# Kernel optimization log

Measured on AMD Instinct MI355X. Metric: run time of the kernel, lower is better.

The kernel has to match this reference:

```python
import jax, jax.numpy as jnp
import numpy as np

B, T, D = 4, 2048, 1024
H, DH = 16, 64
GH = H * DH  # == D here
SCALE = DH ** -0.5
LN_EPS = 1e-5


def setup_inputs() -> dict:
    key = jax.random.key(0)
    ks = jax.random.split(key, 8)
    x = jax.random.normal(ks[0], (B, T, D), dtype=jnp.float32)
    attn_mask = jax.random.uniform(ks[1], (T, T), dtype=jnp.float32)
    # LayerNorm params
    gamma = jnp.ones((D,), jnp.float32)
    beta = jnp.zeros((D,), jnp.float32)
    # projection weights, stored (in, out) so y = x @ W
    Wq = jax.random.normal(ks[2], (D, GH), jnp.float32) * (D ** -0.5)
    Wk = jax.random.normal(ks[3], (D, GH), jnp.float32) * (D ** -0.5)
    Wv = jax.random.normal(ks[4], (D, GH), jnp.float32) * (D ** -0.5)
    Wo = jax.random.normal(ks[5], (GH, D), jnp.float32) * (GH ** -0.5)
    bo = jnp.zeros((D,), jnp.float32)
    return {"x": x, "attn_mask": attn_mask, "gamma": gamma, "beta": beta,
            "Wq": Wq, "Wk": Wk, "Wv": Wv, "Wo": Wo, "bo": bo}


def reference(x, attn_mask, gamma, beta, Wq, Wk, Wv, Wo, bo):
    # LayerNorm over last dim
    mu = jnp.mean(x, axis=-1, keepdims=True)
    var = jnp.mean((x - mu) ** 2, axis=-1, keepdims=True)
    xn = (x - mu) * jax.lax.rsqrt(var + LN_EPS) * gamma + beta
    # QKV projections (bias=False), reshape to [B, H, T, DH]
    split = lambda y: y.reshape(B, T, H, DH).transpose(0, 2, 1, 3)
    q = split(xn @ Wq)
    k = split(xn @ Wk)
    v = split(xn @ Wv)
    # scores scaled then MULTIPLICATIVELY masked (post-scale)
    scores = jnp.einsum('bhqd,bhkd->bhqk', q, k) * SCALE
    scores = scores * attn_mask  # broadcast [T,T] over [B,H,T,T]
    probs = jax.nn.softmax(scores, axis=-1)  # dropout p=0 -> identity
    av = jnp.einsum('bhqk,bhkd->bhqd', probs, v)
    av = av.transpose(0, 2, 1, 3).reshape(B, T, GH)
    return av @ Wo + bo
```

## Files before the change

### kernel.cpp

```cpp
#include <hip/hip_runtime.h>

typedef unsigned short u16;
typedef unsigned int u32;
typedef __bf16 bf16x8 __attribute__((ext_vector_type(8)));
typedef float f32x4 __attribute__((ext_vector_type(4)));

#define AS1 __attribute__((address_space(1)))
#define AS3 __attribute__((address_space(3)))

#define SWZB(x) ((x) ^ ((((x) >> 7) & 7) << 4))

__device__ __forceinline__ float bf2f(u16 u) {
    union { u32 i; float f; } v; v.i = ((u32)u) << 16; return v.f;
}
__device__ __forceinline__ u16 f2bf(float f) {
    union { float f; u32 i; } v; v.f = f;
    u32 i = v.i;
    u32 r = (i + 0x7fffu + ((i >> 16) & 1u)) >> 16;
    return (u16)r;
}
__device__ __forceinline__ u32 cvtpk_bf16(float lo, float hi) {
    u32 r;
    asm("v_cvt_pk_bf16_f32 %0, %1, %2" : "=v"(r) : "v"(lo), "v"(hi));
    return r;
}
__device__ __forceinline__ float fexp2(float x) {
    float r;
    asm("v_exp_f32 %0, %1" : "=v"(r) : "v"(x));
    return r;
}
__device__ __forceinline__ void gload_lds16(const u16* src, u16* dst) {
    __builtin_amdgcn_global_load_lds((const AS1 void*)src, (AS3 void*)dst, 16, 0, 0);
}

__global__ __launch_bounds__(256) void transposeW(const float* __restrict__ Wq,
                                                  const float* __restrict__ Wk,
                                                  const float* __restrict__ Wv,
                                                  const float* __restrict__ Wo,
                                                  u16* __restrict__ WT,
                                                  u16* __restrict__ WoT) {
    __shared__ u16 t[64][65];
    int z = blockIdx.z;
    const float* in = (z == 0) ? Wq : (z == 1) ? Wk : (z == 2) ? Wv : Wo;
    u16* out = (z < 3) ? WT + (size_t)z * 1024 * 1024 : WoT;
    float scale = (z == 0) ? 0.18033688f : 1.0f;
    int c = threadIdx.x & 63, r0 = threadIdx.x >> 6;
    int ib = blockIdx.y * 64, jb = blockIdx.x * 64;
    #pragma unroll
    for (int r = r0; r < 64; r += 4)
        t[r][c] = f2bf(in[(size_t)(ib + r) * 1024 + jb + c] * scale);
    __syncthreads();
    #pragma unroll
    for (int r = r0; r < 64; r += 4) out[(size_t)(jb + r) * 1024 + ib + c] = t[c][r];
}

__global__ __launch_bounds__(256) void ln_kernel(const float* __restrict__ x,
                                                 const float* __restrict__ g,
                                                 const float* __restrict__ bb,
                                                 u16* __restrict__ xn) {
    int row = blockIdx.x;
    int tid = threadIdx.x;
    const float* xr = x + (size_t)row * 1024;
    float4 v = *(const float4*)&xr[tid * 4];
    float f0 = v.x, f1 = v.y, f2 = v.z, f3 = v.w;
    float s = f0 + f1 + f2 + f3;
    float sq = f0 * f0 + f1 * f1 + f2 * f2 + f3 * f3;
    #pragma unroll
    for (int m = 1; m < 64; m <<= 1) { s += __shfl_xor(s, m, 64); sq += __shfl_xor(sq, m, 64); }
    __shared__ float red[8];
    int wid = tid >> 6, lane = tid & 63;
    if (lane == 0) { red[wid] = s; red[4 + wid] = sq; }
    __syncthreads();
    s = red[0] + red[1] + red[2] + red[3];
    sq = red[4] + red[5] + red[6] + red[7];
    float mu = s * (1.f / 1024.f);
    float var = sq * (1.f / 1024.f) - mu * mu;
    float rs = rsqrtf(var + 1e-5f);
    float4 gv = *(const float4*)&g[tid * 4];
    float4 bv = *(const float4*)&bb[tid * 4];
    ushort4 o;
    o.x = f2bf((f0 - mu) * rs * gv.x + bv.x);
    o.y = f2bf((f1 - mu) * rs * gv.y + bv.y);
    o.z = f2bf((f2 - mu) * rs * gv.z + bv.z);
    o.w = f2bf((f3 - mu) * rs * gv.w + bv.w);
    *(ushort4*)&xn[(size_t)row * 1024 + tid * 4] = o;
}

__global__ __launch_bounds__(256) void gemm_bt(const u16* __restrict__ A,
                                               const u16* __restrict__ BT,
                                               u16* __restrict__ C16,
                                               float* __restrict__ C32,
                                               const float* __restrict__ bias,
                                               int K, int ldc, int ext, int nbx,
                                               u16* __restrict__ vTout) {
    __shared__ __align__(16) u16 lA[128 * 32];
    __shared__ __align__(16) u16 lB[128 * 32];
    int bid = blockIdx.x;
    int xcd = bid & 7, loc = bid >> 3;
    int npx = nbx >> 3;
    int n0 = (xcd * npx + loc % npx) * 128;
    int m0 = (loc / npx) * 128;
    int tid = threadIdx.x, lane = tid & 63, wid = tid >> 6;
    int wr = wid >> 1, wc = wid & 1;
    int l4 = lane >> 4, l15 = lane & 15;

    f32x4 acc[4][4] = {};
    int NT = K >> 5;

    auto stage = [&](int kt) {
        int k0 = kt << 5;
        #pragma unroll
        for (int i = 0; i < 2; ++i) {
            int j = wid * 2 + i;
            int row = j * 16 + (lane >> 2);
            int ch = (lane & 3) * 8;
            gload_lds16(A + (size_t)(m0 + row) * K + k0 + ch, &lA[j * 512]);
            gload_lds16(BT + (size_t)(n0 + row) * K + k0 + ch, &lB[j * 512]);
        }
    };
    stage(0);
    for (int kt = 0; kt < NT; ++kt) {
        __syncthreads();
        bf16x8 af[4], bfr[4];
        #pragma unroll
        for (int i = 0; i < 4; ++i) {
            af[i]  = *(const bf16x8*)&lA[(wr * 64 + i * 16 + l15) * 32 + l4 * 8];
            bfr[i] = *(const bf16x8*)&lB[(wc * 64 + i * 16 + l15) * 32 + l4 * 8];
        }
        __syncthreads();
        if (kt + 1 < NT) stage(kt + 1);
        #pragma unroll
        for (int i = 0; i < 4; ++i)
            #pragma unroll
            for (int j = 0; j < 4; ++j)
                acc[i][j] = __builtin_amdgcn_mfma_f32_16x16x32_bf16(af[i], bfr[j], acc[i][j], 0, 0, 0);
    }
    bool vblk = (vTout != nullptr) && (n0 >= 2048);
    #pragma unroll
    for (int j = 0; j < 4; ++j) {
        int col = n0 + wc * 64 + j * 16 + l15;
        if (vblk) {
            int hd = col - 2048;
            #pragma unroll
            for (int i = 0; i < 4; ++i) {
                int trow = m0 + wr * 64 + i * 16 + l4 * 4;
                int bidx = trow >> 11, t = trow & 2047;
                ushort4 pk;
                pk.x = f2bf(acc[i][j][0]);
                pk.y = f2bf(acc[i][j][1]);
                pk.z = f2bf(acc[i][j][2]);
                pk.w = f2bf(acc[i][j][3]);
                *(ushort4*)&vTout[(size_t)(bidx * 1024 + hd) * 2048 + t] = pk;
            }
        } else {
            float bv = ext ? bias[col] : 0.f;
            #pragma unroll
            for (int i = 0; i < 4; ++i) {
                #pragma unroll
                for (int r = 0; r < 4; ++r) {
                    int row = m0 + wr * 64 + i * 16 + l4 * 4 + r;
                    float val = acc[i][j][r] + bv;
                    if (ext) C32[(size_t)row * ldc + col] = val;
                    else     C16[(size_t)row * ldc + col] = f2bf(val);
                }
            }
        }
    }
}

__global__ __launch_bounds__(256) void attn_kernel(const u16* __restrict__ qkv,
                                                   const u16* __restrict__ vT,
                                                   const float* __restrict__ mask,
                                                   u16* __restrict__ av) {
    __shared__ __align__(16) u16 lK[2][64 * 64];
    __shared__ __align__(16) u16 lV[2][64 * 64];
    int qt = blockIdx.x, bh = blockIdx.y;
    int b = bh >> 4, h = bh & 15;
    int tid = threadIdx.x, lane = tid & 63, wid = tid >> 6;
    int l4 = lane >> 4, l15 = lane & 15;
    int qw = qt * 128 + wid * 32;

    const u16* qb0 = qkv + (size_t)(b * 2048 + qw + l15) * 3072 + h * 64;
    const u16* qb1 = qb0 + (size_t)16 * 3072;
    bf16x8 qf00 = *(const bf16x8*)&qb0[l4 * 8];
    bf16x8 qf01 = *(const bf16x8*)&qb0[32 + l4 * 8];
    bf16x8 qf10 = *(const bf16x8*)&qb1[l4 * 8];
    bf16x8 qf11 = *(const bf16x8*)&qb1[32 + l4 * 8];
    const float* mrow0 = mask + (size_t)(qw + l15) * 2048 + 8 * l4;
    const float* mrow1 = mrow0 + (size_t)16 * 2048;

    f32x4 o0[4] = {}, o1[4] = {};
    float lsum0 = 0.f, lsum1 = 0.f;

    int c0 = tid, c1 = 256 + tid;
    auto pmap = [](int g) {
        return (g & 32) + 4 * ((g >> 3) & 3) + (g & 3) + ((g & 4) << 2);
    };
    int kd0 = SWZB(pmap(c0 >> 3) * 128 + (c0 & 7) * 16);
    int kd1 = SWZB(pmap(c1 >> 3) * 128 + (c1 & 7) * 16);
    int vd0 = SWZB((c0 >> 3) * 128 + (c0 & 7) * 16);
    int vd1 = SWZB((c1 >> 3) * 128 + (c1 & 7) * 16);
    const u16* ksrc0 = qkv + (size_t)(b * 2048 + (c0 >> 3)) * 3072 + 1024 + h * 64 + (c0 & 7) * 8;
    const u16* ksrc1 = qkv + (size_t)(b * 2048 + (c1 >> 3)) * 3072 + 1024 + h * 64 + (c1 & 7) * 8;
    const u16* vsrc0 = vT + (size_t)(bh * 64 + (c0 >> 3)) * 2048 + (c0 & 7) * 8;
    const u16* vsrc1 = vT + (size_t)(bh * 64 + (c1 >> 3)) * 2048 + (c1 & 7) * 8;

    auto loadKV = [&](int t, bf16x8& K0, bf16x8& K1, bf16x8& V0, bf16x8& V1) {
        size_t ko = (size_t)t * (64 * 3072);
        int vo = t * 64;
        K0 = *(const bf16x8*)(ksrc0 + ko);
        K1 = *(const bf16x8*)(ksrc1 + ko);
        V0 = *(const bf16x8*)(vsrc0 + vo);
        V1 = *(const bf16x8*)(vsrc1 + vo);
    };

    union PU { u32 u[4]; bf16x8 v; };

    auto body = [&](int t, int pbuf,
                    bf16x8& nK0, bf16x8& nK1, bf16x8& nV0, bf16x8& nV1,
                    bf16x8& fK0, bf16x8& fK1, bf16x8& fV0, bf16x8& fV1) {
        int k0 = t * 64;
        f32x4 mm0[4], mm1[4];
        mm0[0] = *(const f32x4*)(mrow0 + k0);
        mm0[1] = *(const f32x4*)(mrow0 + k0 + 4);
        mm0[2] = *(const f32x4*)(mrow0 + k0 + 32);
        mm0[3] = *(const f32x4*)(mrow0 + k0 + 36);
        mm1[0] = *(const f32x4*)(mrow1 + k0);
        mm1[1] = *(const f32x4*)(mrow1 + k0 + 4);
        mm1[2] = *(const f32x4*)(mrow1 + k0 + 32);
        mm1[3] = *(const f32x4*)(mrow1 + k0 + 36);
        const char* Kb = (const char*)lK[pbuf];
        f32x4 s0[4] = {}, s1[4] = {};
        __builtin_amdgcn_s_setprio(1);
        #pragma unroll
        for (int fj = 0; fj < 4; ++fj) {
            bf16x8 kf0 = *(const bf16x8*)(Kb + SWZB((fj * 16 + l15) * 128 + l4 * 16));
            bf16x8 kf1 = *(const bf16x8*)(Kb + SWZB((fj * 16 + l15) * 128 + 64 + l4 * 16));
            s0[fj] = __builtin_amdgcn_mfma_f32_16x16x32_bf16(kf0, qf00, s0[fj], 0, 0, 0);
            s0[fj] = __builtin_amdgcn_mfma_f32_16x16x32_bf16(kf1, qf01, s0[fj], 0, 0, 0);
            s1[fj] = __builtin_amdgcn_mfma_f32_16x16x32_bf16(kf0, qf10, s1[fj], 0, 0, 0);
            s1[fj] = __builtin_amdgcn_mfma_f32_16x16x32_bf16(kf1, qf11, s1[fj], 0, 0, 0);
        }
        __builtin_amdgcn_s_setprio(0);
        PU pa0[2], pa1[2];
        #pragma unroll
        for (int fj = 0; fj < 4; ++fj) {
            float p0 = fexp2(s0[fj][0] * mm0[fj][0]);
            float p1 = fexp2(s0[fj][1] * mm0[fj][1]);
            float p2 = fexp2(s0[fj][2] * mm0[fj][2]);
            float p3 = fexp2(s0[fj][3] * mm0[fj][3]);
            lsum0 += (p0 + p1) + (p2 + p3);
            int ks = fj >> 1, hf = (fj & 1) * 2;
            pa0[ks].u[hf]     = cvtpk_bf16(p0, p1);
            pa0[ks].u[hf + 1] = cvtpk_bf16(p2, p3);
        }
        #pragma unroll
        for (int fj = 0; fj < 4; ++fj) {
            float p0 = fexp2(s1[fj][0] * mm1[fj][0]);
            float p1 = fexp2(s1[fj][1] * mm1[fj][1]);
            float p2 = fexp2(s1[fj][2] * mm1[fj][2]);
            float p3 = fexp2(s1[fj][3] * mm1[fj][3]);
            lsum1 += (p0 + p1) + (p2 + p3);
            int ks = fj >> 1, hf = (fj & 1) * 2;
            pa1[ks].u[hf]     = cvtpk_bf16(p0, p1);
            pa1[ks].u[hf + 1] = cvtpk_bf16(p2, p3);
        }
        if (t + 1 < 32) {
            char* Kn = (char*)lK[pbuf ^ 1];
            char* Vn = (char*)lV[pbuf ^ 1];
            *(bf16x8*)(Kn + kd0) = nK0;
            *(bf16x8*)(Kn + kd1) = nK1;
            *(bf16x8*)(Vn + vd0) = nV0;
            *(bf16x8*)(Vn + vd1) = nV1;
        }
        if (t + 2 < 32) loadKV(t + 2, fK0, fK1, fV0, fV1);
        const char* Vb = (const char*)lV[pbuf];
        __builtin_amdgcn_s_setprio(1);
        #pragma unroll
        for (int ks = 0; ks < 2; ++ks) {
            #pragma unroll
            for (int fj = 0; fj < 4; ++fj) {
                bf16x8 vf = *(const bf16x8*)(Vb + SWZB((fj * 16 + l15) * 128 + ks * 64 + l4 * 16));
                o0[fj] = __builtin_amdgcn_mfma_f32_16x16x32_bf16(pa0[ks].v, vf, o0[fj], 0, 0, 0);
                o1[fj] = __builtin_amdgcn_mfma_f32_16x16x32_bf16(pa1[ks].v, vf, o1[fj], 0, 0, 0);
            }
        }
        __builtin_amdgcn_s_setprio(0);
        __syncthreads();
    };

    bf16x8 ka0, ka1, va0, va1, kb0, kb1, vb0, vb1;
    loadKV(0, ka0, ka1, va0, va1);
    *(bf16x8*)((char*)lK[0] + kd0) = ka0;
    *(bf16x8*)((char*)lK[0] + kd1) = ka1;
    *(bf16x8*)((char*)lV[0] + vd0) = va0;
    *(bf16x8*)((char*)lV[0] + vd1) = va1;
    loadKV(1, kb0, kb1, vb0, vb1);
    __syncthreads();
    for (int t = 0; t < 32; t += 2) {
        body(t,     0, kb0, kb1, vb0, vb1, ka0, ka1, va0, va1);
        body(t + 1, 1, ka0, ka1, va0, va1, kb0, kb1, vb0, vb1);
    }

    lsum0 += __shfl_xor(lsum0, 16, 64);
    lsum0 += __shfl_xor(lsum0, 32, 64);
    lsum1 += __shfl_xor(lsum1, 16, 64);
    lsum1 += __shfl_xor(lsum1, 32, 64);
    float den0[4], den1[4];
    #pragma unroll
    for (int r = 0; r < 4; ++r) {
        den0[r] = __shfl(lsum0, l4 * 4 + r, 64);
        den1[r] = __shfl(lsum1, l4 * 4 + r, 64);
    }
    #pragma unroll
    for (int fj = 0; fj < 4; ++fj) {
        #pragma unroll
        for (int r = 0; r < 4; ++r) {
            int col = h * 64 + fj * 16 + l15;
            av[(size_t)(b * 2048 + qw + l4 * 4 + r) * 1024 + col]      = f2bf(o0[fj][r] / den0[r]);
            av[(size_t)(b * 2048 + qw + 16 + l4 * 4 + r) * 1024 + col] = f2bf(o1[fj][r] / den1[r]);
        }
    }
}

extern "C" void kernel_launch(void* const* d_in, const int* in_sizes, int n_in,
                              void* d_out, int out_size, void* d_ws, size_t ws_size,
                              hipStream_t stream) {
    (void)in_sizes; (void)n_in; (void)out_size; (void)ws_size;
    const float* x     = (const float*)d_in[0];
    const float* mask  = (const float*)d_in[1];
    const float* gamma = (const float*)d_in[2];
    const float* beta  = (const float*)d_in[3];
    const float* Wq    = (const float*)d_in[4];
    const float* Wk    = (const float*)d_in[5];
    const float* Wv    = (const float*)d_in[6];
    const float* Wo    = (const float*)d_in[7];
    const float* bo    = (const float*)d_in[8];

    char* ws = (char*)d_ws;
    u16* xn   = (u16*)(ws);
    u16* WT   = (u16*)(ws + 16777216);
    u16* WoT  = (u16*)(ws + 16777216 + 6291456);
    u16* qkvb = (u16*)(ws + 16777216 + 6291456 + 2097152);
    u16* vT   = (u16*)(ws + 16777216 + 6291456 + 2097152 + 50331648);
    u16* av = xn;

    dim3 tb(256);
    transposeW<<<dim3(16, 16, 4), tb, 0, stream>>>(Wq, Wk, Wv, Wo, WT, WoT);
    ln_kernel<<<8192, tb, 0, stream>>>(x, gamma, beta, xn);
    gemm_bt<<<24 * 64, tb, 0, stream>>>(xn, WT, qkvb, nullptr, nullptr, 1024, 3072, 0, 24, vT);
    attn_kernel<<<dim3(16, 64), tb, 0, stream>>>(qkvb, vT, mask, av);
    gemm_bt<<<8 * 64, tb, 0, stream>>>(av, WoT, nullptr, (float*)d_out, bo, 1024, 1024, 1, 8, nullptr);
}
```

Measured before the change: 259.7 us.

## Software-pipeline attention: overlap next tile's QK^T with current softmax and PV

Restructures the attention inner loop into a skewed software pipeline in which QK^T for tile t is issued alongside exp/pack and PV for tile t-1. K/V shared-memory buffers go from double to triple buffering so the previous V tile stays live, and score registers alternate between two sets. The goal is to let MFMA work overlap with exp/convert VALU work within a wave. The cost is more LDS and more live registers, which may reduce occupancy or cause spills.

```diff
diff --git a/kernel.cpp b/kernel.cpp
--- a/kernel.cpp
+++ b/kernel.cpp
@@ -172,8 +172,8 @@
                                                    const u16* __restrict__ vT,
                                                    const float* __restrict__ mask,
                                                    u16* __restrict__ av) {
-    __shared__ __align__(16) u16 lK[2][64 * 64];
-    __shared__ __align__(16) u16 lV[2][64 * 64];
+    __shared__ __align__(16) u16 lK[3][64 * 64];
+    __shared__ __align__(16) u16 lV[3][64 * 64];
     int qt = blockIdx.x, bh = blockIdx.y;
     int b = bh >> 4, h = bh & 15;
     int tid = threadIdx.x, lane = tid & 63, wid = tid >> 6;
@@ -216,9 +216,73 @@
 
     union PU { u32 u[4]; bf16x8 v; };
 
-    auto body = [&](int t, int pbuf,
-                    bf16x8& nK0, bf16x8& nK1, bf16x8& nV0, bf16x8& nV1,
-                    bf16x8& fK0, bf16x8& fK1, bf16x8& fV0, bf16x8& fV1) {
+    f32x4 sE0[4], sE1[4], sO0[4], sO1[4];
+    bf16x8 ka0, ka1, va0, va1, kb0, kb1, vb0, vb1;
+
+    auto EXPPA = [&](f32x4 (&sp0)[4], f32x4 (&sp1)[4], PU (&pa0)[2], PU (&pa1)[2]) {
+        #pragma unroll
+        for (int fj = 0; fj < 4; ++fj) {
+            float p0 = fexp2(sp0[fj][0]);
+            float p1 = fexp2(sp0[fj][1]);
+            float p2 = fexp2(sp0[fj][2]);
+            float p3 = fexp2(sp0[fj][3]);
+            lsum0 += (p0 + p1) + (p2 + p3);
+            int ks = fj >> 1, hf = (fj & 1) * 2;
+            pa0[ks].u[hf]     = cvtpk_bf16(p0, p1);
+            pa0[ks].u[hf + 1] = cvtpk_bf16(p2, p3);
+        }
+        #pragma unroll
+        for (int fj = 0; fj < 4; ++fj) {
+            float p0 = fexp2(sp1[fj][0]);
+            float p1 = fexp2(sp1[fj][1]);
+            float p2 = fexp2(sp1[fj][2]);
+            float p3 = fexp2(sp1[fj][3]);
+            lsum1 += (p0 + p1) + (p2 + p3);
+            int ks = fj >> 1, hf = (fj & 1) * 2;
+            pa1[ks].u[hf]     = cvtpk_bf16(p0, p1);
+            pa1[ks].u[hf + 1] = cvtpk_bf16(p2, p3);
+        }
+    };
+    auto PV = [&](const char* Vb, PU (&pa0)[2], PU (&pa1)[2]) {
+        __builtin_amdgcn_s_setprio(1);
+        #pragma unroll
+        for (int ks = 0; ks < 2; ++ks) {
+            #pragma unroll
+            for (int fj = 0; fj < 4; ++fj) {
+                bf16x8 vf = *(const bf16x8*)(Vb + SWZB((fj * 16 + l15) * 128 + ks * 64 + l4 * 16));
+                o0[fj] = __builtin_amdgcn_mfma_f32_16x16x32_bf16(pa0[ks].v, vf, o0[fj], 0, 0, 0);
+                o1[fj] = __builtin_amdgcn_mfma_f32_16x16x32_bf16(pa1[ks].v, vf, o1[fj], 0, 0, 0);
+            }
+        }
+        __builtin_amdgcn_s_setprio(0);
+    };
+    auto QKT = [&](const char* Kb, f32x4 (&sc0)[4], f32x4 (&sc1)[4]) {
+        __builtin_amdgcn_s_setprio(1);
+        #pragma unroll
+        for (int fj = 0; fj < 4; ++fj) {
+            bf16x8 kf0 = *(const bf16x8*)(Kb + SWZB((fj * 16 + l15) * 128 + l4 * 16));
+            bf16x8 kf1 = *(const bf16x8*)(Kb + SWZB((fj * 16 + l15) * 128 + 64 + l4 * 16));
+            f32x4 z0 = {0.f, 0.f, 0.f, 0.f};
+            z0 = __builtin_amdgcn_mfma_f32_16x16x32_bf16(kf0, qf00, z0, 0, 0, 0);
+            sc0[fj] = __builtin_amdgcn_mfma_f32_16x16x32_bf16(kf1, qf01, z0, 0, 0, 0);
+            f32x4 z1 = {0.f, 0.f, 0.f, 0.f};
+            z1 = __builtin_amdgcn_mfma_f32_16x16x32_bf16(kf0, qf10, z1, 0, 0, 0);
+            sc1[fj] = __builtin_amdgcn_mfma_f32_16x16x32_bf16(kf1, qf11, z1, 0, 0, 0);
+        }
+        __builtin_amdgcn_s_setprio(0);
+    };
+    auto STAGE = [&](char* Kd, char* Vd, bf16x8& K0, bf16x8& K1, bf16x8& V0, bf16x8& V1) {
+        *(bf16x8*)(Kd + kd0) = K0;
+        *(bf16x8*)(Kd + kd1) = K1;
+        *(bf16x8*)(Vd + vd0) = V0;
+        *(bf16x8*)(Vd + vd1) = V1;
+    };
+
+    auto step = [&](int t, char* Kcur, char* Vprev, char* Kstg, char* Vstg,
+                    bf16x8& gK0, bf16x8& gK1, bf16x8& gV0, bf16x8& gV1,
+                    bf16x8& fK0, bf16x8& fK1, bf16x8& fV0, bf16x8& fV1,
+                    f32x4 (&sc0)[4], f32x4 (&sc1)[4],
+                    f32x4 (&sp0)[4], f32x4 (&sp1)[4]) {
         int k0 = t * 64;
         f32x4 mm0[4], mm1[4];
         mm0[0] = *(const f32x4*)(mrow0 + k0);
@@ -229,77 +293,61 @@
         mm1[1] = *(const f32x4*)(mrow1 + k0 + 4);
         mm1[2] = *(const f32x4*)(mrow1 + k0 + 32);
         mm1[3] = *(const f32x4*)(mrow1 + k0 + 36);
-        const char* Kb = (const char*)lK[pbuf];
-        f32x4 s0[4] = {}, s1[4] = {};
-        __builtin_amdgcn_s_setprio(1);
+        QKT(Kcur, sc0, sc1);
+        PU pa0[2], pa1[2];
+        EXPPA(sp0, sp1, pa0, pa1);
+        if (t + 1 < 32) STAGE(Kstg, Vstg, gK0, gK1, gV0, gV1);
+        if (t + 2 < 32) loadKV(t + 2, fK0, fK1, fV0, fV1);
+        PV(Vprev, pa0, pa1);
         #pragma unroll
         for (int fj = 0; fj < 4; ++fj) {
-            bf16x8 kf0 = *(const bf16x8*)(Kb + SWZB((fj * 16 + l15) * 128 + l4 * 16));
-            bf16x8 kf1 = *(const bf16x8*)(Kb + SWZB((fj * 16 + l15) * 128 + 64 + l4 * 16));
-            s0[fj] = __builtin_amdgcn_mfma_f32_16x16x32_bf16(kf0, qf00, s0[fj], 0, 0, 0);
-            s0[fj] = __builtin_amdgcn_mfma_f32_16x16x32_bf16(kf1, qf01, s0[fj], 0, 0, 0);
-            s1[fj] = __builtin_amdgcn_mfma_f32_16x16x32_bf16(kf0, qf10, s1[fj], 0, 0, 0);
-            s1[fj] = __builtin_amdgcn_mfma_f32_16x16x32_bf16(kf1, qf11, s1[fj], 0, 0, 0);
-        }
-        __builtin_amdgcn_s_setprio(0);
-        PU pa0[2], pa1[2];
-        #pragma unroll
-        for (int fj = 0; fj < 4; ++fj) {
-            float p0 = fexp2(s0[fj][0] * mm0[fj][0]);
-            float p1 = fexp2(s0[fj][1] * mm0[fj][1]);
-            float p2 = fexp2(s0[fj][2] * mm0[fj][2]);
-            float p3 = fexp2(s0[fj][3] * mm0[fj][3]);
-            lsum0 += (p0 + p1) + (p2 + p3);
-            int ks = fj >> 1, hf = (fj & 1) * 2;
-            pa0[ks].u[hf]     = cvtpk_bf16(p0, p1);
-            pa0[ks].u[hf + 1] = cvtpk_bf16(p2, p3);
-        }
-        #pragma unroll
-        for (int fj = 0; fj < 4; ++fj) {
-            float p0 = fexp2(s1[fj][0] * mm1[fj][0]);
-            float p1 = fexp2(s1[fj][1] * mm1[fj][1]);
-            float p2 = fexp2(s1[fj][2] * mm1[fj][2]);
-            float p3 = fexp2(s1[fj][3] * mm1[fj][3]);
-            lsum1 += (p0 + p1) + (p2 + p3);
-            int ks = fj >> 1, hf = (fj & 1) * 2;
-            pa1[ks].u[hf]     = cvtpk_bf16(p0, p1);
-            pa1[ks].u[hf + 1] = cvtpk_bf16(p2, p3);
-        }
-        if (t + 1 < 32) {
-            char* Kn = (char*)lK[pbuf ^ 1];
-            char* Vn = (char*)lV[pbuf ^ 1];
-            *(bf16x8*)(Kn + kd0) = nK0;
-            *(bf16x8*)(Kn + kd1) = nK1;
-            *(bf16x8*)(Vn + vd0) = nV0;
-            *(bf16x8*)(Vn + vd1) = nV1;
-        }
-        if (t + 2 < 32) loadKV(t + 2, fK0, fK1, fV0, fV1);
-        const char* Vb = (const char*)lV[pbuf];
-        __builtin_amdgcn_s_setprio(1);
-        #pragma unroll
-        for (int ks = 0; ks < 2; ++ks) {
-            #pragma unroll
-            for (int fj = 0; fj < 4; ++fj) {
-                bf16x8 vf = *(const bf16x8*)(Vb + SWZB((fj * 16 + l15) * 128 + ks * 64 + l4 * 16));
-                o0[fj] = __builtin_amdgcn_mfma_f32_16x16x32_bf16(pa0[ks].v, vf, o0[fj], 0, 0, 0);
-                o1[fj] = __builtin_amdgcn_mfma_f32_16x16x32_bf16(pa1[ks].v, vf, o1[fj], 0, 0, 0);
-            }
-        }
-        __builtin_amdgcn_s_setprio(0);
+            sc0[fj] *= mm0[fj];
+            sc1[fj] *= mm1[fj];
+        }
         __syncthreads();
     };
 
-    bf16x8 ka0, ka1, va0, va1, kb0, kb1, vb0, vb1;
     loadKV(0, ka0, ka1, va0, va1);
-    *(bf16x8*)((char*)lK[0] + kd0) = ka0;
-    *(bf16x8*)((char*)lK[0] + kd1) = ka1;
-    *(bf16x8*)((char*)lV[0] + vd0) = va0;
-    *(bf16x8*)((char*)lV[0] + vd1) = va1;
+    STAGE((char*)lK[0], (char*)lV[0], ka0, ka1, va0, va1);
     loadKV(1, kb0, kb1, vb0, vb1);
     __syncthreads();
-    for (int t = 0; t < 32; t += 2) {
-        body(t,     0, kb0, kb1, vb0, vb1, ka0, ka1, va0, va1);
-        body(t + 1, 1, ka0, ka1, va0, va1, kb0, kb1, vb0, vb1);
+    {
+        f32x4 mm0[4], mm1[4];
+        mm0[0] = *(const f32x4*)(mrow0);
+        mm0[1] = *(const f32x4*)(mrow0 + 4);
+        mm0[2] = *(const f32x4*)(mrow0 + 32);
+        mm0[3] = *(const f32x4*)(mrow0 + 36);
+        mm1[0] = *(const f32x4*)(mrow1);
+        mm1[1] = *(const f32x4*)(mrow1 + 4);
+        mm1[2] = *(const f32x4*)(mrow1 + 32);
+        mm1[3] = *(const f32x4*)(mrow1 + 36);
+        QKT((const char*)lK[0], sE0, sE1);
+        STAGE((char*)lK[1], (char*)lV[1], kb0, kb1, vb0, vb1);
+        loadKV(2, ka0, ka1, va0, va1);
+        #pragma unroll
+        for (int fj = 0; fj < 4; ++fj) { sE0[fj] *= mm0[fj]; sE1[fj] *= mm1[fj]; }
+        __syncthreads();
+    }
+    step(1, (char*)lK[1], (char*)lV[0], (char*)lK[2], (char*)lV[2],
+         ka0, ka1, va0, va1, kb0, kb1, vb0, vb1, sO0, sO1, sE0, sE1);
+    for (int i0 = 2; i0 < 32; i0 += 6) {
+        step(i0 + 0, (char*)lK[2], (char*)lV[1], (char*)lK[0], (char*)lV[0],
+             kb0, kb1, vb0, vb1, ka0, ka1, va0, va1, sE0, sE1, sO0, sO1);
+        step(i0 + 1, (char*)lK[0], (char*)lV[2], (char*)lK[1], (char*)lV[1],
+             ka0, ka1, va0, va1, kb0, kb1, vb0, vb1, sO0, sO1, sE0, sE1);
+        step(i0 + 2, (char*)lK[1], (char*)lV[0], (char*)lK[2], (char*)lV[2],
+             kb0, kb1, vb0, vb1, ka0, ka1, va0, va1, sE0, sE1, sO0, sO1);
+        step(i0 + 3, (char*)lK[2], (char*)lV[1], (char*)lK[0], (char*)lV[0],
+             ka0, ka1, va0, va1, kb0, kb1, vb0, vb1, sO0, sO1, sE0, sE1);
+        step(i0 + 4, (char*)lK[0], (char*)lV[2], (char*)lK[1], (char*)lV[1],
+             kb0, kb1, vb0, vb1, ka0, ka1, va0, va1, sE0, sE1, sO0, sO1);
+        step(i0 + 5, (char*)lK[1], (char*)lV[0], (char*)lK[2], (char*)lV[2],
+             ka0, ka1, va0, va1, kb0, kb1, vb0, vb1, sO0, sO1, sE0, sE1);
+    }
+    {
+        PU pa0[2], pa1[2];
+        EXPPA(sO0, sO1, pa0, pa1);
+        PV((const char*)lV[1], pa0, pa1);
     }
 
     lsum0 += __shfl_xor(lsum0, 16, 64);
```

Result: slower. 274.8 us (+5.8%).
